# Optimization experiments

Measured on AMD Instinct MI355X. Metric: run time of the kernel, lower is better.

The kernel has to match this reference:

```python
import jax, jax.numpy as jnp
import numpy as np

B, TE, TD, HE, HD = 8, 256, 128, 512, 512


def setup_inputs() -> dict:
    key = jax.random.key(0)
    k1, k2, k3, k4, k5 = jax.random.split(key, 5)
    # scale weights down (original uses 'uniform' init) to keep tanh unsaturated
    return {
        "encoder_out_seq": jax.random.normal(k1, (B, TE, HE), dtype=jnp.float32),
        "decoder_out_seq": jax.random.normal(k2, (B, TD, HD), dtype=jnp.float32),
        "W_a": jax.random.normal(k3, (HE, HE), dtype=jnp.float32) * 0.05,
        "U_a": jax.random.normal(k4, (HD, HE), dtype=jnp.float32) * 0.05,
        "V_a": jax.random.normal(k5, (HE, 1), dtype=jnp.float32) * 0.05,
    }


def reference(encoder_out_seq, decoder_out_seq, W_a, U_a, V_a):
    # Bahdanau additive attention, vectorized over all decoder timesteps
    # (the original loops over Td via K.rnn; steps are independent).
    Ws = jnp.einsum('bte,eh->bth', encoder_out_seq, W_a)   # [B, Te, He]
    Uh = jnp.einsum('bdk,kh->bdh', decoder_out_seq, U_a)   # [B, Td, He]
    # tanh(S.Wa + h.Ua): broadcast to [B, Td, Te, He], contract with V_a
    act = jnp.tanh(Ws[:, None, :, :] + Uh[:, :, None, :])  # [B, Td, Te, He]
    e = jnp.einsum('bdth,ho->bdt', act, V_a)                # [B, Td, Te]
    e = jax.nn.softmax(e, axis=-1)                          # attention weights
    c = jnp.einsum('bdt,bth->bdh', e, encoder_out_seq)      # [B, Td, He] contexts
    return (c, e)
```

## Files before the change

kernel.cpp:

```cpp
#include <hip/hip_runtime.h>

#define B_  8
#define TE_ 256
#define TD_ 128
#define HE_ 512

typedef __attribute__((ext_vector_type(8))) short short8v;
typedef __attribute__((ext_vector_type(4))) float f32x4;

__global__ __launch_bounds__(512) void gemm_fused(
    const float* __restrict__ enc, const float* __restrict__ dec,
    const float* __restrict__ Wa, const float* __restrict__ Ua,
    float* __restrict__ C) {
  __shared__ short BT[2][32][512];
  const int bid = blockIdx.x;
  const int mt = bid % 24, nt = bid / 24;
  const int m0 = mt * 128, n0 = nt * 32;
  const float* Bsrc = (mt < 16) ? Wa : Ua;
  const float* Asrc = (mt < 16) ? enc + (size_t)m0 * 512
                                : dec + (size_t)(m0 - 2048) * 512;
  const int tid = threadIdx.x;
  {
    const int kp = tid >> 3;
    const int c4 = (tid & 7) * 4;
    for (int p = 0; p < 4; ++p) {
      const int k = 2 * kp + p * 128;
      float4 v0 = *(const float4*)(Bsrc + (size_t)k * 512 + n0 + c4);
      float4 v1 = *(const float4*)(Bsrc + (size_t)(k + 1) * 512 + n0 + c4);
      const float a0[4] = {v0.x, v0.y, v0.z, v0.w};
      const float a1[4] = {v1.x, v1.y, v1.z, v1.w};
      const int kc = k >> 3, klo = k & 7;
#pragma unroll
      for (int q = 0; q < 4; ++q) {
        const int n = c4 + q;
        unsigned u0 = __float_as_uint(a0[q]);
        unsigned u1 = __float_as_uint(a1[q]);
        unsigned hi32 = __builtin_amdgcn_perm(u1, u0, 0x07060302);
        float l0 = a0[q] - __uint_as_float(u0 & 0xffff0000u);
        float l1 = a1[q] - __uint_as_float(u1 & 0xffff0000u);
        unsigned lo32 = __builtin_amdgcn_perm(__float_as_uint(l1), __float_as_uint(l0), 0x07060302);
        const int slot = (kc & ~7) | ((kc ^ n) & 7);
        *(unsigned*)&BT[0][n][slot * 8 + klo] = hi32;
        *(unsigned*)&BT[1][n][slot * 8 + klo] = lo32;
      }
    }
  }
  __syncthreads();
  const int w = tid >> 6, lane = tid & 63;
  const int fm = lane & 15, fc = lane >> 4;
  const float* Ap = Asrc + (size_t)(w * 16 + fm) * 512 + fc * 8;
  f32x4 acc0 = {}, acc1 = {};
  float4 pfa[2], pfb[2];
  pfa[0] = *(const float4*)(Ap);
  pfb[0] = *(const float4*)(Ap + 4);
  pfa[1] = *(const float4*)(Ap + 32);
  pfb[1] = *(const float4*)(Ap + 36);
  for (int it = 0; it < 16; ++it) {
    const float4 fa = pfa[it & 1];
    const float4 fb = pfb[it & 1];
    if (it < 14) {
      pfa[it & 1] = *(const float4*)(Ap + (it + 2) * 32);
      pfb[it & 1] = *(const float4*)(Ap + (it + 2) * 32 + 4);
    }
    const float af[8] = {fa.x, fa.y, fa.z, fa.w, fb.x, fb.y, fb.z, fb.w};
    union { unsigned u[4]; short8v s; } ahu, alu;
#pragma unroll
    for (int e = 0; e < 4; ++e) {
      unsigned u0 = __float_as_uint(af[2 * e]);
      unsigned u1 = __float_as_uint(af[2 * e + 1]);
      ahu.u[e] = __builtin_amdgcn_perm(u1, u0, 0x07060302);
      float l0 = af[2 * e]     - __uint_as_float(u0 & 0xffff0000u);
      float l1 = af[2 * e + 1] - __uint_as_float(u1 & 0xffff0000u);
      alu.u[e] = __builtin_amdgcn_perm(__float_as_uint(l1), __float_as_uint(l0), 0x07060302);
    }
    const short8v ah = ahu.s, al = alu.s;
    const int kc = it * 4 + fc;
    const int base = kc & ~7;
    const int s0 = (base | ((kc ^ fm) & 7)) * 8;
    const int s1 = (base | ((kc ^ (16 + fm)) & 7)) * 8;
    short8v bh0 = *(const short8v*)&BT[0][fm][s0];
    short8v bl0 = *(const short8v*)&BT[1][fm][s0];
    short8v bh1 = *(const short8v*)&BT[0][16 + fm][s1];
    short8v bl1 = *(const short8v*)&BT[1][16 + fm][s1];
    acc0 = __builtin_amdgcn_mfma_f32_16x16x32_bf16(ah, bh0, acc0, 0, 0, 0);
    acc1 = __builtin_amdgcn_mfma_f32_16x16x32_bf16(ah, bh1, acc1, 0, 0, 0);
    acc0 = __builtin_amdgcn_mfma_f32_16x16x32_bf16(ah, bl0, acc0, 0, 0, 0);
    acc1 = __builtin_amdgcn_mfma_f32_16x16x32_bf16(ah, bl1, acc1, 0, 0, 0);
    acc0 = __builtin_amdgcn_mfma_f32_16x16x32_bf16(al, bh0, acc0, 0, 0, 0);
    acc1 = __builtin_amdgcn_mfma_f32_16x16x32_bf16(al, bh1, acc1, 0, 0, 0);
  }
  const int row = m0 + w * 16 + fc * 4;
  float* Cp = C + (size_t)row * 512 + n0 + fm;
#pragma unroll
  for (int r = 0; r < 4; ++r) Cp[(size_t)r * 512] = acc0[r];
#pragma unroll
  for (int r = 0; r < 4; ++r) Cp[(size_t)r * 512 + 16] = acc1[r];
}

#define C2 2.8853900817779268f
__global__ __launch_bounds__(1024) void attn_fused(
    const float* __restrict__ Ws, const float* __restrict__ Uh,
    const float* __restrict__ Va, const float* __restrict__ enc,
    float* __restrict__ c_out, float* __restrict__ e_out) {
  __shared__ float sUh[4][HE_];
  __shared__ float sV[HE_];
  __shared__ float sE[4][TE_];
  __shared__ float sRed[16];
  __shared__ float sNorm[4];
  const int tid = threadIdx.x;
  const int b  = blockIdx.x & 7;
  const int d0 = (blockIdx.x >> 3) * 4;
  if (tid < 512)
    ((float4*)sUh)[tid] = ((const float4*)(Uh + (size_t)(b * TD_ + d0) * HE_))[tid];
  else if (tid < 640)
    ((float4*)sV)[tid - 512] = ((const float4*)Va)[tid - 512];
  __syncthreads();
  const int lane = tid & 63, w = tid >> 6;
  const int tb = w * 16;
  const int h0 = lane * 8;
  float eU[4][8], vv2[8], sumv = 0.f;
#pragma unroll
  for (int j = 0; j < 8; ++j) {
    const float vj = sV[h0 + j];
    sumv += vj;
    vv2[j] = 2.0f * vj;
#pragma unroll
    for (int d = 0; d < 4; ++d)
      eU[d][j] = __builtin_amdgcn_exp2f(C2 * sUh[d][h0 + j]);
  }
  const float* pw = Ws + ((size_t)b * TE_ + tb) * HE_ + h0;
  float4 a0 = *(const float4*)(pw);
  float4 a1 = *(const float4*)(pw + 4);
  float s0, s1, s2, s3;
#define TELT4(X, J) { \
    float EW = __builtin_amdgcn_exp2f(C2 * (X)); \
    float E0 = EW * eU[0][J], E1 = EW * eU[1][J]; \
    float E2 = EW * eU[2][J], E3 = EW * eU[3][J]; \
    float r0 = __builtin_amdgcn_rcpf(E0 + 1.0f); \
    float r1 = __builtin_amdgcn_rcpf(E1 + 1.0f); \
    float r2 = __builtin_amdgcn_rcpf(E2 + 1.0f); \
    float r3 = __builtin_amdgcn_rcpf(E3 + 1.0f); \
    s0 = fmaf(-vv2[J], r0, s0); s1 = fmaf(-vv2[J], r1, s1); \
    s2 = fmaf(-vv2[J], r2, s2); s3 = fmaf(-vv2[J], r3, s3); }
  for (int ti = 0; ti < 16; ++ti) {
    const float* pn = pw + HE_;
    float4 n0 = *(const float4*)(pn);
    float4 n1 = *(const float4*)(pn + 4);
    s0 = s1 = s2 = s3 = sumv;
    TELT4(a0.x, 0) TELT4(a0.y, 1) TELT4(a0.z, 2) TELT4(a0.w, 3)
    TELT4(a1.x, 4) TELT4(a1.y, 5) TELT4(a1.z, 6) TELT4(a1.w, 7)
#pragma unroll
    for (int off = 32; off; off >>= 1) {
      s0 += __shfl_down(s0, off, 64);
      s1 += __shfl_down(s1, off, 64);
      s2 += __shfl_down(s2, off, 64);
      s3 += __shfl_down(s3, off, 64);
    }
    if (lane == 0) {
      sE[0][tb + ti] = s0; sE[1][tb + ti] = s1;
      sE[2][tb + ti] = s2; sE[3][tb + ti] = s3;
    }
    a0 = n0; a1 = n1;
    pw = pn;
  }
  __syncthreads();
  const int dA = tid >> 8, t = tid & 255;
  const float ex = __expf(sE[dA][t]);
  float sum = ex;
#pragma unroll
  for (int off = 32; off; off >>= 1) sum += __shfl_down(sum, off, 64);
  if (lane == 0) sRed[w] = sum;
  __syncthreads();
  if (tid < 4)
    sNorm[tid] = 1.0f / (sRed[tid * 4] + sRed[tid * 4 + 1] + sRed[tid * 4 + 2] + sRed[tid * 4 + 3]);
  __syncthreads();
  const float wgt = ex * sNorm[dA];
  sE[dA][t] = wgt;
  e_out[(size_t)(b * TD_ + d0 + dA) * TE_ + t] = wgt;
  __syncthreads();
  const int h = tid & 511;
  const int db = (tid >> 9) * 2;
  float a0c = 0.f, a1c = 0.f;
  const float* ep = enc + (size_t)b * TE_ * HE_ + h;
  const float* e0 = sE[db];
  const float* e1 = sE[db + 1];
#pragma unroll 4
  for (int tt = 0; tt < TE_; ++tt) {
    const float ev = ep[(size_t)tt * HE_];
    a0c = fmaf(e0[tt], ev, a0c);
    a1c = fmaf(e1[tt], ev, a1c);
  }
  float* cp = c_out + (size_t)(b * TD_ + d0 + db) * HE_ + h;
  cp[0]   = a0c;
  cp[HE_] = a1c;
}

extern "C" void kernel_launch(void* const* d_in, const int* in_sizes, int n_in,
                              void* d_out, int out_size, void* d_ws, size_t ws_size,
                              hipStream_t stream) {
  const float* enc = (const float*)d_in[0];
  const float* dec = (const float*)d_in[1];
  const float* Wa  = (const float*)d_in[2];
  const float* Ua  = (const float*)d_in[3];
  const float* Va  = (const float*)d_in[4];
  float* c_out = (float*)d_out;
  float* e_out = c_out + (size_t)B_ * TD_ * HE_;
  float* Cws = (float*)d_ws;
  const float* Ws = Cws;
  const float* Uh = Cws + (size_t)2048 * 512;
  gemm_fused<<<384, 512, 0, stream>>>(enc, dec, Wa, Ua, Cws);
  attn_fused<<<256, 1024, 0, stream>>>(Ws, Uh, Va, enc, c_out, e_out);
}
```

Measured before the change: 126.5 us.

## Shrink GEMM tiles, deepen A prefetch ring, use DPP wave reductions

The projection GEMM now uses 64-row tiles with 256-thread blocks, doubling the block count to 768, and each thread stages 8 columns of the B tile. The A-operand prefetch grows from a double buffer to a three-deep ring. The attention kernel replaces shuffle-down reductions with DPP row-shift/broadcast adds, reading the total from lane 63. In exchange, each B tile is converted into LDS by twice as many blocks, and the DPP sequence must stay correct for wave64.

```diff
diff --git a/kernel.cpp b/kernel.cpp
--- a/kernel.cpp
+++ b/kernel.cpp
@@ -8,31 +8,46 @@
 typedef __attribute__((ext_vector_type(8))) short short8v;
 typedef __attribute__((ext_vector_type(4))) float f32x4;
 
-__global__ __launch_bounds__(512) void gemm_fused(
+__device__ __forceinline__ float wave_red_add(float s) {
+#define DPPADD(CTRL) \
+  s += __int_as_float(__builtin_amdgcn_update_dpp(0, __float_as_int(s), CTRL, 0xf, 0xf, true))
+  DPPADD(0x111);
+  DPPADD(0x112);
+  DPPADD(0x114);
+  DPPADD(0x118);
+  DPPADD(0x142);
+  DPPADD(0x143);
+#undef DPPADD
+  return s;
+}
+
+__global__ __launch_bounds__(256) void gemm_fused(
     const float* __restrict__ enc, const float* __restrict__ dec,
     const float* __restrict__ Wa, const float* __restrict__ Ua,
     float* __restrict__ C) {
   __shared__ short BT[2][32][512];
   const int bid = blockIdx.x;
-  const int mt = bid % 24, nt = bid / 24;
-  const int m0 = mt * 128, n0 = nt * 32;
-  const float* Bsrc = (mt < 16) ? Wa : Ua;
-  const float* Asrc = (mt < 16) ? enc + (size_t)m0 * 512
+  const int mt = bid % 48, nt = bid / 48;
+  const int m0 = mt * 64, n0 = nt * 32;
+  const float* Bsrc = (mt < 32) ? Wa : Ua;
+  const float* Asrc = (mt < 32) ? enc + (size_t)m0 * 512
                                 : dec + (size_t)(m0 - 2048) * 512;
   const int tid = threadIdx.x;
   {
-    const int kp = tid >> 3;
-    const int c4 = (tid & 7) * 4;
+    const int kr = tid >> 2;
+    const int c8 = (tid & 3) * 8;
     for (int p = 0; p < 4; ++p) {
-      const int k = 2 * kp + p * 128;
-      float4 v0 = *(const float4*)(Bsrc + (size_t)k * 512 + n0 + c4);
-      float4 v1 = *(const float4*)(Bsrc + (size_t)(k + 1) * 512 + n0 + c4);
-      const float a0[4] = {v0.x, v0.y, v0.z, v0.w};
-      const float a1[4] = {v1.x, v1.y, v1.z, v1.w};
+      const int k = 2 * (kr + p * 64);
+      float4 v00 = *(const float4*)(Bsrc + (size_t)k * 512 + n0 + c8);
+      float4 v01 = *(const float4*)(Bsrc + (size_t)k * 512 + n0 + c8 + 4);
+      float4 v10 = *(const float4*)(Bsrc + (size_t)(k + 1) * 512 + n0 + c8);
+      float4 v11 = *(const float4*)(Bsrc + (size_t)(k + 1) * 512 + n0 + c8 + 4);
+      const float a0[8] = {v00.x, v00.y, v00.z, v00.w, v01.x, v01.y, v01.z, v01.w};
+      const float a1[8] = {v10.x, v10.y, v10.z, v10.w, v11.x, v11.y, v11.z, v11.w};
       const int kc = k >> 3, klo = k & 7;
 #pragma unroll
-      for (int q = 0; q < 4; ++q) {
-        const int n = c4 + q;
+      for (int q = 0; q < 8; ++q) {
+        const int n = c8 + q;
         unsigned u0 = __float_as_uint(a0[q]);
         unsigned u1 = __float_as_uint(a1[q]);
         unsigned hi32 = __builtin_amdgcn_perm(u1, u0, 0x07060302);
@@ -50,17 +65,19 @@
   const int fm = lane & 15, fc = lane >> 4;
   const float* Ap = Asrc + (size_t)(w * 16 + fm) * 512 + fc * 8;
   f32x4 acc0 = {}, acc1 = {};
-  float4 pfa[2], pfb[2];
-  pfa[0] = *(const float4*)(Ap);
-  pfb[0] = *(const float4*)(Ap + 4);
-  pfa[1] = *(const float4*)(Ap + 32);
-  pfb[1] = *(const float4*)(Ap + 36);
+  float4 pfa[3], pfb[3];
+#pragma unroll
+  for (int q = 0; q < 3; ++q) {
+    pfa[q] = *(const float4*)(Ap + q * 32);
+    pfb[q] = *(const float4*)(Ap + q * 32 + 4);
+  }
   for (int it = 0; it < 16; ++it) {
-    const float4 fa = pfa[it & 1];
-    const float4 fb = pfb[it & 1];
-    if (it < 14) {
-      pfa[it & 1] = *(const float4*)(Ap + (it + 2) * 32);
-      pfb[it & 1] = *(const float4*)(Ap + (it + 2) * 32 + 4);
+    const int ring = it % 3;
+    const float4 fa = pfa[ring];
+    const float4 fb = pfb[ring];
+    if (it < 13) {
+      pfa[ring] = *(const float4*)(Ap + (it + 3) * 32);
+      pfb[ring] = *(const float4*)(Ap + (it + 3) * 32 + 4);
     }
     const float af[8] = {fa.x, fa.y, fa.z, fa.w, fb.x, fb.y, fb.z, fb.w};
     union { unsigned u[4]; short8v s; } ahu, alu;
@@ -149,14 +166,11 @@
     s0 = s1 = s2 = s3 = sumv;
     TELT4(a0.x, 0) TELT4(a0.y, 1) TELT4(a0.z, 2) TELT4(a0.w, 3)
     TELT4(a1.x, 4) TELT4(a1.y, 5) TELT4(a1.z, 6) TELT4(a1.w, 7)
-#pragma unroll
-    for (int off = 32; off; off >>= 1) {
-      s0 += __shfl_down(s0, off, 64);
-      s1 += __shfl_down(s1, off, 64);
-      s2 += __shfl_down(s2, off, 64);
-      s3 += __shfl_down(s3, off, 64);
-    }
-    if (lane == 0) {
+    s0 = wave_red_add(s0);
+    s1 = wave_red_add(s1);
+    s2 = wave_red_add(s2);
+    s3 = wave_red_add(s3);
+    if (lane == 63) {
       sE[0][tb + ti] = s0; sE[1][tb + ti] = s1;
       sE[2][tb + ti] = s2; sE[3][tb + ti] = s3;
     }
@@ -166,10 +180,8 @@
   __syncthreads();
   const int dA = tid >> 8, t = tid & 255;
   const float ex = __expf(sE[dA][t]);
-  float sum = ex;
-#pragma unroll
-  for (int off = 32; off; off >>= 1) sum += __shfl_down(sum, off, 64);
-  if (lane == 0) sRed[w] = sum;
+  float sum = wave_red_add(ex);
+  if (lane == 63) sRed[w] = sum;
   __syncthreads();
   if (tid < 4)
     sNorm[tid] = 1.0f / (sRed[tid * 4] + sRed[tid * 4 + 1] + sRed[tid * 4 + 2] + sRed[tid * 4 + 3]);
@@ -208,6 +220,6 @@
   float* Cws = (float*)d_ws;
   const float* Ws = Cws;
   const float* Uh = Cws + (size_t)2048 * 512;
-  gemm_fused<<<384, 512, 0, stream>>>(enc, dec, Wa, Ua, Cws);
+  gemm_fused<<<768, 256, 0, stream>>>(enc, dec, Wa, Ua, Cws);
   attn_fused<<<256, 1024, 0, stream>>>(Ws, Uh, Va, enc, c_out, e_out);
 }
```

Measured after the change: 127.0 us. About the same (+0.3%).
